# Kernel optimization log

Hardware: AMD Instinct MI355X
Metric: run time of the kernel (lower is better)

Reference implementation:

```python
import jax, jax.numpy as jnp
import numpy as np

V, L, D, C = 50000, 512, 300, 128
KS = (3, 4, 5)
B = 64


def setup_inputs() -> dict:
    key = jax.random.key(0)
    ks = jax.random.split(key, 12)
    inp = {
        "x": jax.random.randint(ks[0], (B, L), 0, V),
        "embed_w": jax.random.normal(ks[1], (V, D), jnp.float32) * 0.1,
        "conv_w": jax.random.normal(ks[2], (C, D), jnp.float32) * 0.05,
        "conv_b": jax.random.normal(ks[3], (C,), jnp.float32) * 0.05,
        "fc3_w": jax.random.normal(ks[4], (L - 3,), jnp.float32) * 0.04,
        "fc3_b": jax.random.normal(ks[5], (1,), jnp.float32) * 0.04,
        "fc4_w": jax.random.normal(ks[6], (L - 4,), jnp.float32) * 0.04,
        "fc4_b": jax.random.normal(ks[7], (1,), jnp.float32) * 0.04,
        "fc5_w": jax.random.normal(ks[8], (L - 5,), jnp.float32) * 0.04,
        "fc5_b": jax.random.normal(ks[9], (1,), jnp.float32) * 0.04,
        "fc_w": jax.random.normal(ks[10], (C, C * len(KS)), jnp.float32) * 0.05,
        "fc_b": jax.random.normal(ks[11], (C,), jnp.float32) * 0.05,
    }
    return inp


def reference(x, embed_w, conv_w, conv_b, fc3_w, fc3_b, fc4_w, fc4_b,
              fc5_w, fc5_b, fc_w, fc_b):
    # Embedding lookup: [B, L, D]
    emb = embed_w[x]
    # Exclusive prefix sum over the sequence dim (O(L) sliding sums).
    cs = jnp.concatenate(
        [jnp.zeros_like(emb[:, :1]), jnp.cumsum(emb, axis=1)], axis=1)  # [B, L+1, D]
    fcs = ((fc3_w, fc3_b), (fc4_w, fc4_b), (fc5_w, fc5_b))
    outs = []
    for k, (wk, bk) in zip(KS, fcs):
        # Window i sums tokens i..i+k-1; only L-k windows (range(L-k) in original).
        win = cs[:, k:L] - cs[:, :L - k]                      # [B, L-k, D]
        # conv_sim: dot each window-sum against C label vectors (kernel (1, D)).
        sim = jnp.einsum('bld,cd->bcl', win, conv_w) + conv_b[None, :, None]
        # Dropout is identity in eval; fcs[k]: Linear(L-k, 1) shared across channels.
        outs.append(jnp.einsum('bcl,l->bc', sim, wk) + bk)    # [B, C]
    h = jnp.concatenate(outs, axis=1)                          # [B, C*3]
    return h @ fc_w.T + fc_b                                   # [B, C]
```

## Files before the change

### kernel.cpp

```cpp
#include <hip/hip_runtime.h>
#include <stdint.h>

#define BB 64
#define LL 512
#define DD 300
#define CC 128

#define OFF_GRED  (BB * 32 * 3 * DD)
#define OFF_W2    (OFF_GRED + BB * 3 * DD)
#define OFF_BIAS2 (OFF_W2 + CC * 3 * DD)

__global__ __launch_bounds__(256) void k_gather(
    const int* __restrict__ x, const float* __restrict__ embed,
    const float* __restrict__ conv_w, const float* __restrict__ conv_b,
    const float* __restrict__ w3, const float* __restrict__ b3,
    const float* __restrict__ w4, const float* __restrict__ b4,
    const float* __restrict__ w5, const float* __restrict__ b5,
    const float* __restrict__ fcw, const float* __restrict__ fcb,
    float* __restrict__ Gpart, float* __restrict__ W2,
    float* __restrict__ bias2) {
  const int blk = blockIdx.x;
  const int tid = threadIdx.x;

  if (blk < 1024) {
    const int b = blk >> 4;
    const int tc = blk & 15;
    const int sub = tid >> 7;
    const int stid = tid & 127;

    __shared__ int sx[32];
    __shared__ float su[3][32];

    if (tid < 32) {
      const int t = tc * 32 + tid;
      sx[tid] = x[b * LL + t];
      const float* ws[3] = {w3, w4, w5};
#pragma unroll
      for (int kk = 0; kk < 3; ++kk) {
        const int k = kk + 3;
        int lo = t - k + 1; if (lo < 0) lo = 0;
        int hi = t; const int lim = LL - k - 1; if (hi > lim) hi = lim;
        float s = 0.f;
        for (int l = lo; l <= hi; ++l) s += ws[kk][l];
        su[kk][tid] = s;
      }
    }
    __syncthreads();

    float a0x = 0.f, a0y = 0.f, a1x = 0.f, a1y = 0.f, a2x = 0.f, a2y = 0.f;
    float c0x = 0.f, c0y = 0.f, c1x = 0.f, c1y = 0.f, c2x = 0.f, c2y = 0.f;
    const bool tail = stid < (DD / 2 - 128);

#pragma unroll
    for (int half = 0; half < 2; ++half) {
      const int base = sub * 16 + half * 8;
      float2 v[8], u[8];
#pragma unroll
      for (int i = 0; i < 8; ++i) {
        const float2* rp = (const float2*)(embed + (size_t)sx[base + i] * DD);
        v[i] = rp[stid];
      }
      if (tail) {
#pragma unroll
        for (int i = 0; i < 8; ++i) {
          const float2* rp =
              (const float2*)(embed + (size_t)sx[base + i] * DD);
          u[i] = rp[128 + stid];
        }
      }
#pragma unroll
      for (int i = 0; i < 8; ++i) {
        const int j = base + i;
        const float w0 = su[0][j], w1 = su[1][j], w2 = su[2][j];
        a0x += w0 * v[i].x; a0y += w0 * v[i].y;
        a1x += w1 * v[i].x; a1y += w1 * v[i].y;
        a2x += w2 * v[i].x; a2y += w2 * v[i].y;
        if (tail) {
          c0x += w0 * u[i].x; c0y += w0 * u[i].y;
          c1x += w1 * u[i].x; c1y += w1 * u[i].y;
          c2x += w2 * u[i].x; c2y += w2 * u[i].y;
        }
      }
    }

    const int p = tc * 2 + sub;
    float* Gp = Gpart + (size_t)(b * 32 + p) * (3 * DD);
    const int d0 = 2 * stid;
    Gp[0 * DD + d0] = a0x; Gp[0 * DD + d0 + 1] = a0y;
    Gp[1 * DD + d0] = a1x; Gp[1 * DD + d0 + 1] = a1y;
    Gp[2 * DD + d0] = a2x; Gp[2 * DD + d0 + 1] = a2y;
    if (tail) {
      const int d1 = 2 * (128 + stid);
      Gp[0 * DD + d1] = c0x; Gp[0 * DD + d1 + 1] = c0y;
      Gp[1 * DD + d1] = c1x; Gp[1 * DD + d1 + 1] = c1y;
      Gp[2 * DD + d1] = c2x; Gp[2 * DD + d1 + 1] = c2y;
    }
  } else if (blk < 1504) {
    const int w = (blk - 1024) * 4 + (tid >> 6);
    const int lane = tid & 63;
    const int c = w / 15;
    const int rem = w - c * 15;
    const int kk = rem / 5;
    const int chunk = rem - kk * 5;
    const int d = chunk * 64 + lane;
    if (d < DD) {
      const float* fr = fcw + c * (3 * CC) + kk * CC;
      float acc0 = 0.f, acc1 = 0.f;
#pragma unroll 4
      for (int cp = 0; cp < CC; cp += 2) {
        acc0 += fr[cp] * conv_w[cp * DD + d];
        acc1 += fr[cp + 1] * conv_w[(cp + 1) * DD + d];
      }
      W2[c * (3 * DD) + kk * DD + d] = acc0 + acc1;
    }
  } else {
    const int wid = tid >> 6;
    const int lane = tid & 63;
    const int c = (blk - 1504) * 4 + wid;
    float sk[3];
    const float* ws[3] = {w3, w4, w5};
#pragma unroll
    for (int kk = 0; kk < 3; ++kk) {
      const int len = LL - (kk + 3);
      float s = 0.f;
      for (int l = lane; l < len; l += 64) s += ws[kk][l];
#pragma unroll
      for (int off = 32; off >= 1; off >>= 1) s += __shfl_down(s, off, 64);
      sk[kk] = __shfl(s, 0, 64);
    }
    const float bkv[3] = {b3[0], b4[0], b5[0]};
    float acc = 0.f;
#pragma unroll
    for (int s6 = 0; s6 < 6; ++s6) {
      const int j = s6 * 64 + lane;
      const int kk = j >> 7;
      const int cp = j & 127;
      acc += fcw[c * (3 * CC) + j] * (conv_b[cp] * sk[kk] + bkv[kk]);
    }
#pragma unroll
    for (int off = 32; off >= 1; off >>= 1) acc += __shfl_down(acc, off, 64);
    if (lane == 0) bias2[c] = acc + fcb[c];
  }
}

__global__ __launch_bounds__(256) void k_reduce(
    const float* __restrict__ Gpart, float* __restrict__ Gred) {
  const int gid = blockIdx.x * 256 + threadIdx.x;
  const int out = gid >> 2;
  const int r = gid & 3;
  const int b = out / 225;
  const int q = out - b * 225;
  const float4* gp =
      (const float4*)Gpart + (size_t)b * 32 * 225 + (size_t)r * 8 * 225 + q;
  float4 s = gp[0];
#pragma unroll
  for (int p = 1; p < 8; ++p) {
    const float4 v = gp[(size_t)p * 225];
    s.x += v.x; s.y += v.y; s.z += v.z; s.w += v.w;
  }
#pragma unroll
  for (int off = 1; off <= 2; off <<= 1) {
    s.x += __shfl_down(s.x, off, 64);
    s.y += __shfl_down(s.y, off, 64);
    s.z += __shfl_down(s.z, off, 64);
    s.w += __shfl_down(s.w, off, 64);
  }
  if (r == 0) ((float4*)Gred)[out] = s;
}

__global__ __launch_bounds__(256) void k_out(
    const float* __restrict__ Gred, const float* __restrict__ W2,
    const float* __restrict__ bias2, float* __restrict__ out) {
  const int o = blockIdx.x * 4 + (threadIdx.x >> 6);
  const int lane = threadIdx.x & 63;
  const int b = o >> 7;
  const int c = o & 127;

  const float2* wr = (const float2*)(W2 + c * (3 * DD));
  const float2* gr = (const float2*)(Gred + b * (3 * DD));
  float acc = 0.f;
#pragma unroll
  for (int s = 0; s < 7; ++s) {
    const float2 v = wr[s * 64 + lane];
    const float2 g = gr[s * 64 + lane];
    acc += v.x * g.x + v.y * g.y;
  }
  if (lane < 2) {
    const float2 v = wr[448 + lane];
    const float2 g = gr[448 + lane];
    acc += v.x * g.x + v.y * g.y;
  }
#pragma unroll
  for (int off = 32; off >= 1; off >>= 1) acc += __shfl_down(acc, off, 64);
  if (lane == 0) out[b * CC + c] = acc + bias2[c];
}

extern "C" void kernel_launch(void* const* d_in, const int* in_sizes, int n_in,
                              void* d_out, int out_size, void* d_ws,
                              size_t ws_size, hipStream_t stream) {
  const int* x = (const int*)d_in[0];
  const float* embed = (const float*)d_in[1];
  const float* conv_w = (const float*)d_in[2];
  const float* conv_b = (const float*)d_in[3];
  const float* fc3w = (const float*)d_in[4];
  const float* fc3b = (const float*)d_in[5];
  const float* fc4w = (const float*)d_in[6];
  const float* fc4b = (const float*)d_in[7];
  const float* fc5w = (const float*)d_in[8];
  const float* fc5b = (const float*)d_in[9];
  const float* fcw = (const float*)d_in[10];
  const float* fcb = (const float*)d_in[11];

  float* Gpart = (float*)d_ws;
  float* Gred = (float*)d_ws + OFF_GRED;
  float* W2 = (float*)d_ws + OFF_W2;
  float* bias2 = (float*)d_ws + OFF_BIAS2;

  k_gather<<<dim3(1536), dim3(256), 0, stream>>>(
      x, embed, conv_w, conv_b, fc3w, fc3b, fc4w, fc4b, fc5w, fc5b, fcw, fcb,
      Gpart, W2, bias2);
  k_reduce<<<dim3(225), dim3(256), 0, stream>>>(Gpart, Gred);
  k_out<<<dim3(2048), dim3(256), 0, stream>>>(Gred, W2, bias2,
                                              (float*)d_out);
}
```

Measured before the change: 129.4 us.

## Fuse partial-sum reduction into output kernel via shared memory

Merges the k_reduce and k_out kernels into one k_redout kernel. Each block reduces the 32 partial G rows for one batch element into shared memory and then computes 32 output channels, two per wave iteration. This removes one kernel launch and the global round trip for Gred. In exchange, each of the four blocks per batch repeats the 32-way reduction, and the reduction runs serially over 32 loads per thread.

After: 129.0 us (median of 2 runs). No clear change (-0.3%).

```diff
diff --git a/kernel.cpp b/kernel.cpp
--- a/kernel.cpp
+++ b/kernel.cpp
@@ -143,56 +143,60 @@
   }
 }
 
-__global__ __launch_bounds__(256) void k_reduce(
-    const float* __restrict__ Gpart, float* __restrict__ Gred) {
-  const int gid = blockIdx.x * 256 + threadIdx.x;
-  const int out = gid >> 2;
-  const int r = gid & 3;
-  const int b = out / 225;
-  const int q = out - b * 225;
-  const float4* gp =
-      (const float4*)Gpart + (size_t)b * 32 * 225 + (size_t)r * 8 * 225 + q;
-  float4 s = gp[0];
-#pragma unroll
-  for (int p = 1; p < 8; ++p) {
-    const float4 v = gp[(size_t)p * 225];
-    s.x += v.x; s.y += v.y; s.z += v.z; s.w += v.w;
+__global__ __launch_bounds__(256) void k_redout(
+    const float* __restrict__ Gpart, const float* __restrict__ W2,
+    const float* __restrict__ bias2, float* __restrict__ out) {
+  const int b = blockIdx.x >> 2;
+  const int cgrp = blockIdx.x & 3;
+  const int tid = threadIdx.x;
+  __shared__ float gred[3 * DD];
+
+  if (tid < 225) {
+    const float4* gp = (const float4*)Gpart + (size_t)b * 32 * 225 + tid;
+    float4 s = gp[0];
+#pragma unroll
+    for (int p = 1; p < 32; ++p) {
+      const float4 v = gp[(size_t)p * 225];
+      s.x += v.x; s.y += v.y; s.z += v.z; s.w += v.w;
+    }
+    ((float4*)gred)[tid] = s;
   }
-#pragma unroll
-  for (int off = 1; off <= 2; off <<= 1) {
-    s.x += __shfl_down(s.x, off, 64);
-    s.y += __shfl_down(s.y, off, 64);
-    s.z += __shfl_down(s.z, off, 64);
-    s.w += __shfl_down(s.w, off, 64);
+  __syncthreads();
+
+  const int w = tid >> 6;
+  const int lane = tid & 63;
+  const float2* gr = (const float2*)gred;
+#pragma unroll
+  for (int pair = 0; pair < 4; ++pair) {
+    const int c0 = cgrp * 32 + w * 8 + pair * 2;
+    const float2* wr0 = (const float2*)(W2 + c0 * (3 * DD));
+    const float2* wr1 = (const float2*)(W2 + (c0 + 1) * (3 * DD));
+    float a0 = 0.f, a1 = 0.f;
+#pragma unroll
+    for (int s = 0; s < 7; ++s) {
+      const float2 g = gr[s * 64 + lane];
+      const float2 va = wr0[s * 64 + lane];
+      const float2 vb = wr1[s * 64 + lane];
+      a0 += va.x * g.x + va.y * g.y;
+      a1 += vb.x * g.x + vb.y * g.y;
+    }
+    if (lane < 2) {
+      const float2 g = gr[448 + lane];
+      const float2 va = wr0[448 + lane];
+      const float2 vb = wr1[448 + lane];
+      a0 += va.x * g.x + va.y * g.y;
+      a1 += vb.x * g.x + vb.y * g.y;
+    }
+#pragma unroll
+    for (int off = 32; off >= 1; off >>= 1) {
+      a0 += __shfl_down(a0, off, 64);
+      a1 += __shfl_down(a1, off, 64);
+    }
+    if (lane == 0) {
+      out[b * CC + c0] = a0 + bias2[c0];
+      out[b * CC + c0 + 1] = a1 + bias2[c0 + 1];
+    }
   }
-  if (r == 0) ((float4*)Gred)[out] = s;
-}
-
-__global__ __launch_bounds__(256) void k_out(
-    const float* __restrict__ Gred, const float* __restrict__ W2,
-    const float* __restrict__ bias2, float* __restrict__ out) {
-  const int o = blockIdx.x * 4 + (threadIdx.x >> 6);
-  const int lane = threadIdx.x & 63;
-  const int b = o >> 7;
-  const int c = o & 127;
-
-  const float2* wr = (const float2*)(W2 + c * (3 * DD));
-  const float2* gr = (const float2*)(Gred + b * (3 * DD));
-  float acc = 0.f;
-#pragma unroll
-  for (int s = 0; s < 7; ++s) {
-    const float2 v = wr[s * 64 + lane];
-    const float2 g = gr[s * 64 + lane];
-    acc += v.x * g.x + v.y * g.y;
-  }
-  if (lane < 2) {
-    const float2 v = wr[448 + lane];
-    const float2 g = gr[448 + lane];
-    acc += v.x * g.x + v.y * g.y;
-  }
-#pragma unroll
-  for (int off = 32; off >= 1; off >>= 1) acc += __shfl_down(acc, off, 64);
-  if (lane == 0) out[b * CC + c] = acc + bias2[c];
 }
 
 extern "C" void kernel_launch(void* const* d_in, const int* in_sizes, int n_in,
@@ -212,14 +216,12 @@
   const float* fcb = (const float*)d_in[11];
 
   float* Gpart = (float*)d_ws;
-  float* Gred = (float*)d_ws + OFF_GRED;
   float* W2 = (float*)d_ws + OFF_W2;
   float* bias2 = (float*)d_ws + OFF_BIAS2;
 
   k_gather<<<dim3(1536), dim3(256), 0, stream>>>(
       x, embed, conv_w, conv_b, fc3w, fc3b, fc4w, fc4b, fc5w, fc5b, fcw, fcb,
       Gpart, W2, bias2);
-  k_reduce<<<dim3(225), dim3(256), 0, stream>>>(Gpart, Gred);
-  k_out<<<dim3(2048), dim3(256), 0, stream>>>(Gred, W2, bias2,
-                                              (float*)d_out);
+  k_redout<<<dim3(256), dim3(256), 0, stream>>>(Gpart, W2, bias2,
+                                                (float*)d_out);
 }
```
